# Performance work log

Measured on AMD Instinct MI355X. Metric: run time of the kernel, lower is better.

## Reference

```python
import jax, jax.numpy as jnp
import numpy as np

B, NC, C, H, L = 256, 99, 128, 512, 3
N = NC + 1              # nodes per graph (depot + customers)
NT = B * N              # total nodes
EPS = 1e-5


def _edge_index():
    # PyG-style: torch.combinations(arange(n), r=2) -> directed upper-tri edges, replicated per batch
    r, c = np.triu_indices(N, k=1)
    offs = (np.arange(B) * N)[:, None]
    row = (r[None, :] + offs).ravel()
    col = (c[None, :] + offs).ravel()
    # gcn_norm adds self loops
    sl = np.arange(NT)
    row = np.concatenate([row, sl])
    col = np.concatenate([col, sl])
    return jnp.asarray(row, jnp.int32), jnp.asarray(col, jnp.int32)


def _bn(x, g, b):
    # BatchNorm1d in training mode over flattened (B*n, C); biased variance
    m = x.mean(0)
    v = jnp.mean((x - m) ** 2, axis=0)
    return g * (x - m) * jax.lax.rsqrt(v + EPS) + b


def setup_inputs() -> dict:
    key = jax.random.key(0)
    ks = jax.random.split(key, 16)
    f = jax.random.normal
    return dict(
        depot_xy=jax.random.uniform(ks[0], (B, 2), jnp.float32),
        customer_xy=jax.random.uniform(ks[1], (B, NC, 2), jnp.float32),
        demand=jax.random.uniform(ks[2], (B, NC), jnp.float32),
        W_depot=f(ks[3], (2, C), jnp.float32) * 0.5,
        b_depot=f(ks[4], (C,), jnp.float32) * 0.1,
        W_init=f(ks[5], (3, C), jnp.float32) * 0.5,
        b_init=f(ks[6], (C,), jnp.float32) * 0.1,
        gcn_W=f(ks[7], (L, C, C), jnp.float32) / np.sqrt(C),
        gcn_b=f(ks[8], (L, C), jnp.float32) * 0.1,
        bn_gamma=jnp.ones((L, C), jnp.float32),
        bn_beta=jnp.zeros((L, C), jnp.float32),
        ff_W1=f(ks[9], (L, C, H), jnp.float32) / np.sqrt(C),
        ff_b1=f(ks[10], (L, H), jnp.float32) * 0.1,
        ff_W2=f(ks[11], (L, H, C), jnp.float32) / np.sqrt(H),
        ff_b2=f(ks[12], (L, C), jnp.float32) * 0.1,
    )


def reference(depot_xy, customer_xy, demand, W_depot, b_depot, W_init, b_init,
              gcn_W, gcn_b, bn_gamma, bn_beta, ff_W1, ff_b1, ff_W2, ff_b2):
    # initial node embeddings
    depot_e = depot_xy @ W_depot + b_depot                      # [B, C]
    cust_in = jnp.concatenate([customer_xy, demand[..., None]], -1)  # [B, NC, 3]
    cust_e = cust_in @ W_init + b_init                          # [B, NC, C]
    x = jnp.concatenate([depot_e[:, None, :], cust_e], 1).reshape(NT, C)

    row, col = _edge_index()
    # GCN symmetric normalization (with self loops, directed src->dst)
    deg = jax.ops.segment_sum(jnp.ones_like(col, x.dtype), col, num_segments=NT)
    dis = jnp.where(deg > 0, jax.lax.rsqrt(deg), 0.0)
    norm = dis[row] * dis[col]                                  # [E]

    for l in range(L):
        h = x @ gcn_W[l]                                        # [NT, C]
        msg = norm[:, None] * h[row]                            # gather + scale
        agg = jax.ops.segment_sum(msg, col, num_segments=NT) + gcn_b[l]
        x = _bn(x + agg, bn_gamma[l], bn_beta[l])
        ff = jax.nn.relu(x @ ff_W1[l] + ff_b1[l]) @ ff_W2[l] + ff_b2[l]
        x = _bn(x + ff, bn_gamma[l], bn_beta[l])

    nodes = x.reshape(B, N, C)
    return nodes, jnp.mean(nodes, axis=1)
```

## Files before the change

### kernel.cpp

```cpp
#include <hip/hip_runtime.h>

constexpr int kB = 256;
constexpr int kNC = 99;
constexpr int kN = 100;
constexpr int kC = 128;
constexpr int kH = 512;
constexpr int kL = 3;
constexpr int kNT = kB * kN;
constexpr int kRT = 64;
constexpr int kFFBlocks = kNT / kRT;
constexpr float kEps = 1e-5f;

typedef unsigned short u16;
typedef unsigned int u32;
typedef __attribute__((ext_vector_type(8))) __bf16 bf16x8;
typedef __attribute__((ext_vector_type(4))) float f32x4;
typedef __attribute__((ext_vector_type(8))) unsigned short u16x8;

__device__ __forceinline__ u16 f2bf(float x) {
  __bf16 h = (__bf16)x;
  return __builtin_bit_cast(u16, h);
}
__device__ __forceinline__ float bf2f(u16 h) {
  union { u32 u; float f; } v; v.u = ((u32)h) << 16;
  return v.f;
}

__device__ __forceinline__ void affine_from_stats(
    const float* __restrict__ stats, const float* __restrict__ gamma,
    const float* __restrict__ beta, int c, float& sc, float& sh) {
  if (stats != nullptr) {
    float s = stats[c], sq = stats[kC + c];
    float m = s * (1.0f / kNT);
    float v = sq * (1.0f / kNT) - m * m;
    float rs = rsqrtf(v + kEps);
    sc = gamma[c] * rs;
    sh = beta[c] - m * sc;
  } else {
    sc = 1.0f;
    sh = 0.0f;
  }
}

__device__ __forceinline__ void pack_group(
    int g, const float* __restrict__ gcnW, const float* __restrict__ W1,
    const float* __restrict__ W2, u16* __restrict__ wpack) {
  int layer = g / 36864, r = g % 36864;
  const float* src; int shf; u16* base; int isW2 = 0;
  if (r < 4096) {
    src = gcnW + (size_t)layer * kC * kC; shf = 7;
    base = wpack + (size_t)(layer * 288 + 0) * 512;
  } else if (r < 20480) {
    src = W1 + (size_t)layer * kC * kH; shf = 9;
    base = wpack + (size_t)(layer * 288 + 32) * 512; r -= 4096;
  } else {
    src = W2 + (size_t)layer * kH * kC; shf = 7;
    base = wpack + (size_t)(layer * 288 + 160) * 512; r -= 20480; isW2 = 1;
  }
  int e4 = r * 4;
  int k = e4 >> shf, n0 = e4 & ((1 << shf) - 1);
  float4 v = *(const float4*)(src + ((size_t)k << shf) + n0);
  float vv[4] = {v.x, v.y, v.z, v.w};
  int kb = k >> 5, hi = (k >> 3) & 3, j = k & 7;
#pragma unroll
  for (int t = 0; t < 4; ++t) {
    int n = n0 + t;
    int nb = n >> 4, l = hi * 16 + (n & 15);
    int f = isW2 ? (nb * 16 + kb) : (nb * 4 + kb);
    base[(size_t)f * 512 + l * 8 + j] = f2bf(vv[t]);
  }
}

template <bool FIRST>
__global__ __launch_bounds__(256) void k_gcn(
    const u16* __restrict__ yprev, const float* __restrict__ stats_prev,
    const float* __restrict__ gamma_p, const float* __restrict__ beta_p,
    const u16* __restrict__ Wgp, const float* __restrict__ gb,
    float* __restrict__ stats_out, u16* __restrict__ yA,
    const float* __restrict__ dxy, const float* __restrict__ cxy,
    const float* __restrict__ dem, const float* __restrict__ Wd,
    const float* __restrict__ bd, const float* __restrict__ Wi,
    const float* __restrict__ bi, const float* __restrict__ gcnW,
    const float* __restrict__ W1, const float* __restrict__ W2,
    u16* __restrict__ wpack) {
  __shared__ float s_scale[kC], s_shift[kC];
  __shared__ u16 xs[112][136];
  __shared__ float hs[kN][68];
  __shared__ float sP[4][64], s_sum[64], s_sq[64];
  __shared__ float scoord[kN][4];
  __shared__ float swt[7][kC];
  const int tid = threadIdx.x;
  const int b = blockIdx.x >> 1, half = blockIdx.x & 1;
  const int wave = tid >> 6, lane = tid & 63;
  const int arow = lane & 15, kofs = (lane >> 4) * 8;
  const int crow = (lane >> 4) * 4, ccol = lane & 15;
  const int nbW = half * 4 + wave;
  bf16x8 bfr[4];
  if (FIRST) {
#pragma unroll
    for (int kb = 0; kb < 4; ++kb)
#pragma unroll
      for (int e = 0; e < 8; ++e) {
        int krow = kb * 32 + (lane >> 4) * 8 + e;
        bfr[kb][e] = (__bf16)gcnW[(size_t)krow * kC + nbW * 16 + (lane & 15)];
      }
  } else {
#pragma unroll
    for (int kb = 0; kb < 4; ++kb)
      bfr[kb] = *(const bf16x8*)(Wgp + (size_t)(nbW * 4 + kb) * 512 + lane * 8);
  }
  if (FIRST) {
    int g = blockIdx.x * 256 + tid;
    if (g < kL * 36864) pack_group(g, gcnW, W1, W2, wpack);
    if (tid < kN) {
      if (tid == 0) {
        scoord[0][0] = dxy[b * 2];
        scoord[0][1] = dxy[b * 2 + 1];
        scoord[0][2] = 0.0f;
      } else {
        int q = b * kNC + tid - 1;
        scoord[tid][0] = cxy[q * 2];
        scoord[tid][1] = cxy[q * 2 + 1];
        scoord[tid][2] = dem[q];
      }
    }
    if (tid < 224) {
      int f = tid * 4, r = f >> 7, c = f & 127;
      const float* s;
      switch (r) {
        case 0: s = Wd + c; break;
        case 1: s = Wd + kC + c; break;
        case 2: s = bd + c; break;
        case 3: s = Wi + c; break;
        case 4: s = Wi + kC + c; break;
        case 5: s = Wi + 2 * kC + c; break;
        default: s = bi + c; break;
      }
      *(float4*)&swt[r][c] = *(const float4*)s;
    }
  }
  if (tid < kC) affine_from_stats(stats_prev, gamma_p, beta_p, tid,
                                  s_scale[tid], s_shift[tid]);
  if (tid < 64) { s_sum[tid] = 0.0f; s_sq[tid] = 0.0f; }
  __syncthreads();
  const size_t gbase = (size_t)b * kN * kC;
#pragma unroll
  for (int i = 0; i < 14; ++i) {
    int li = i * 256 + tid;
    int lr = li >> 5, lc = (li & 31) * 4;
    float g0 = 0.f, g1 = 0.f, g2 = 0.f, g3 = 0.f;
    if (lr < kN) {
      if (FIRST) {
        float sx = scoord[lr][0], sy = scoord[lr][1], sd = scoord[lr][2];
        if (lr == 0) {
          g0 = fmaf(sx, swt[0][lc + 0], fmaf(sy, swt[1][lc + 0], swt[2][lc + 0]));
          g1 = fmaf(sx, swt[0][lc + 1], fmaf(sy, swt[1][lc + 1], swt[2][lc + 1]));
          g2 = fmaf(sx, swt[0][lc + 2], fmaf(sy, swt[1][lc + 2], swt[2][lc + 2]));
          g3 = fmaf(sx, swt[0][lc + 3], fmaf(sy, swt[1][lc + 3], swt[2][lc + 3]));
        } else {
          g0 = fmaf(sx, swt[3][lc + 0],
                    fmaf(sy, swt[4][lc + 0], fmaf(sd, swt[5][lc + 0], swt[6][lc + 0])));
          g1 = fmaf(sx, swt[3][lc + 1],
                    fmaf(sy, swt[4][lc + 1], fmaf(sd, swt[5][lc + 1], swt[6][lc + 1])));
          g2 = fmaf(sx, swt[3][lc + 2],
                    fmaf(sy, swt[4][lc + 2], fmaf(sd, swt[5][lc + 2], swt[6][lc + 2])));
          g3 = fmaf(sx, swt[3][lc + 3],
                    fmaf(sy, swt[4][lc + 3], fmaf(sd, swt[5][lc + 3], swt[6][lc + 3])));
        }
      } else {
        ushort4 hv = *(const ushort4*)(yprev + gbase + (size_t)lr * kC + lc);
        g0 = bf2f(hv.x); g1 = bf2f(hv.y); g2 = bf2f(hv.z); g3 = bf2f(hv.w);
      }
    }
    ushort4 h4;
    h4.x = f2bf(fmaf(g0, s_scale[lc + 0], s_shift[lc + 0]));
    h4.y = f2bf(fmaf(g1, s_scale[lc + 1], s_shift[lc + 1]));
    h4.z = f2bf(fmaf(g2, s_scale[lc + 2], s_shift[lc + 2]));
    h4.w = f2bf(fmaf(g3, s_scale[lc + 3], s_shift[lc + 3]));
    *(ushort4*)&xs[lr][lc] = h4;
  }
  __syncthreads();
  {
#pragma unroll
    for (int t = 0; t < 7; ++t) {
      f32x4 acc = {0.f, 0.f, 0.f, 0.f};
#pragma unroll
      for (int kb = 0; kb < 4; ++kb) {
        bf16x8 a = *(const bf16x8*)&xs[t * 16 + arow][kb * 32 + kofs];
        acc = __builtin_amdgcn_mfma_f32_16x16x32_bf16(a, bfr[kb], acc, 0, 0, 0);
      }
      int rbase = t * 16 + crow;
#pragma unroll
      for (int r = 0; r < 4; ++r)
        if (rbase + r < kN) hs[rbase + r][wave * 16 + ccol] = acc[r];
    }
  }
  __syncthreads();
  const int c = tid & 63, jh = tid >> 6;
  const int ch = half * 64 + c;
  const float sc = s_scale[ch], sh = s_shift[ch];
  const float gbc = gb[ch];
  const int j0 = jh * 25;
  float p = 0.0f;
#pragma unroll
  for (int jj = 0; jj < 25; ++jj)
    p = fmaf(hs[j0 + jj][c], rsqrtf((float)(j0 + jj + 1)), p);
  sP[jh][c] = p;
  __syncthreads();
  float s = 0.0f;
  for (int q = 0; q < jh; ++q) s += sP[q][c];
  float wv0 = 0.f, wv1 = 0.f, wv2 = 0.f, wv3 = 0.f, wd0 = 0.f, wd1 = 0.f, wd2 = 0.f;
  if (FIRST) {
    wv0 = swt[3][ch]; wv1 = swt[4][ch]; wv2 = swt[5][ch]; wv3 = swt[6][ch];
    wd0 = swt[0][ch]; wd1 = swt[1][ch]; wd2 = swt[2][ch];
  }
  float lsum = 0.0f, lsq = 0.0f;
#pragma unroll
  for (int jj = 0; jj < 25; ++jj) {
    int j = j0 + jj;
    float r = rsqrtf((float)(j + 1));
    s = fmaf(hs[j][c], r, s);
    float xv;
    if (FIRST) {
      float sx = scoord[j][0], sy = scoord[j][1], sd = scoord[j][2];
      xv = (j == 0) ? fmaf(sx, wd0, fmaf(sy, wd1, wd2))
                    : fmaf(sx, wv0, fmaf(sy, wv1, fmaf(sd, wv2, wv3)));
    } else {
      xv = fmaf(bf2f(yprev[gbase + (size_t)j * kC + ch]), sc, sh);
    }
    float yv = xv + fmaf(s, r, gbc);
    yA[gbase + (size_t)j * kC + ch] = f2bf(yv);
    lsum += yv;
    lsq = fmaf(yv, yv, lsq);
  }
  atomicAdd(&s_sum[c], lsum);
  atomicAdd(&s_sq[c], lsq);
  __syncthreads();
  if (tid < 64) {
    atomicAdd(&stats_out[half * 64 + tid], s_sum[tid]);
    atomicAdd(&stats_out[kC + half * 64 + tid], s_sq[tid]);
  }
}

template <bool LAST>
__global__ __launch_bounds__(512, 2) void k_ff(
    const u16* __restrict__ yA, const float* __restrict__ stats_in,
    const float* __restrict__ gamma, const float* __restrict__ beta,
    const u16* __restrict__ W1p, const float* __restrict__ b1,
    const u16* __restrict__ W2p, const float* __restrict__ b2,
    float* __restrict__ stats_out, u16* __restrict__ yB16,
    float* __restrict__ yB32) {
  __shared__ float s_scale[kC], s_shift[kC], s_sum[kC], s_sq[kC];
  __shared__ float s_b1[kH];
  __shared__ u16 xs[kRT][136];
  __shared__ u16 hid[kRT][136];
  const int tid = threadIdx.x;
  const int wave = tid >> 6, lane = tid & 63;
  const int arow = lane & 15, kofs = (lane >> 4) * 8;
  const int crow = (lane >> 4) * 4, ccol = lane & 15;
  if (tid < kC) {
    affine_from_stats(stats_in, gamma, beta, tid, s_scale[tid], s_shift[tid]);
    s_sum[tid] = 0.0f;
    s_sq[tid] = 0.0f;
  }
  if (tid < 128) ((float4*)s_b1)[tid] = ((const float4*)b1)[tid];
  __syncthreads();
  const int rb = blockIdx.x * kRT;
#pragma unroll
  for (int i = 0; i < 2; ++i) {
    int li = i * 512 + tid;
    int lr = li >> 4, lc8 = (li & 15) * 8;
    u16x8 hv = *(const u16x8*)(yA + (size_t)(rb + lr) * kC + lc8);
    u16x8 o;
#pragma unroll
    for (int e = 0; e < 8; ++e)
      o[e] = f2bf(fmaf(bf2f(hv[e]), s_scale[lc8 + e], s_shift[lc8 + e]));
    *(u16x8*)&xs[lr][lc8] = o;
  }
  const int c = wave * 16 + ccol;
  u16 resid[16];
#pragma unroll
  for (int rt = 0; rt < 4; ++rt)
#pragma unroll
    for (int r = 0; r < 4; ++r)
      resid[rt * 4 + r] = yA[(size_t)(rb + rt * 16 + crow + r) * kC + c];
  __syncthreads();

  f32x4 oacc[4] = {{0.f, 0.f, 0.f, 0.f}, {0.f, 0.f, 0.f, 0.f},
                   {0.f, 0.f, 0.f, 0.f}, {0.f, 0.f, 0.f, 0.f}};
  for (int chk = 0; chk < 4; ++chk) {
    bf16x8 bw[4];
#pragma unroll
    for (int kb = 0; kb < 4; ++kb)
      bw[kb] = *(const bf16x8*)(W2p + (size_t)(wave * 16 + chk * 4 + kb) * 512 + lane * 8);
    const int nb = chk * 8 + wave;
    bf16x8 b1f[4];
#pragma unroll
    for (int kb = 0; kb < 4; ++kb)
      b1f[kb] = *(const bf16x8*)(W1p + (size_t)(nb * 4 + kb) * 512 + lane * 8);
    const float bbias = s_b1[chk * 128 + c];
#pragma unroll
    for (int rt = 0; rt < 4; ++rt) {
      f32x4 acc = {0.f, 0.f, 0.f, 0.f};
#pragma unroll
      for (int kb = 0; kb < 4; ++kb) {
        bf16x8 a = *(const bf16x8*)&xs[rt * 16 + arow][kb * 32 + kofs];
        acc = __builtin_amdgcn_mfma_f32_16x16x32_bf16(a, b1f[kb], acc, 0, 0, 0);
      }
#pragma unroll
      for (int r = 0; r < 4; ++r)
        hid[rt * 16 + crow + r][c] = f2bf(fmaxf(acc[r] + bbias, 0.0f));
    }
    __syncthreads();
#pragma unroll
    for (int kb = 0; kb < 4; ++kb) {
#pragma unroll
      for (int rt = 0; rt < 4; ++rt) {
        bf16x8 ha = *(const bf16x8*)&hid[rt * 16 + arow][kb * 32 + kofs];
        oacc[rt] = __builtin_amdgcn_mfma_f32_16x16x32_bf16(ha, bw[kb], oacc[rt], 0, 0, 0);
      }
    }
    __syncthreads();
  }

  const float sc = s_scale[c], sh = s_shift[c], bb = b2[c];
  float psum = 0.0f, psq = 0.0f;
#pragma unroll
  for (int rt = 0; rt < 4; ++rt) {
#pragma unroll
    for (int r = 0; r < 4; ++r) {
      int lrow = rt * 16 + crow + r;
      float xv = fmaf(bf2f(resid[rt * 4 + r]), sc, sh);
      float o = oacc[rt][r] + bb + xv;
      if (LAST)
        yB32[(size_t)(rb + lrow) * kC + c] = o;
      else
        yB16[(size_t)(rb + lrow) * kC + c] = f2bf(o);
      psum += o;
      psq = fmaf(o, o, psq);
    }
  }
  atomicAdd(&s_sum[c], psum);
  atomicAdd(&s_sq[c], psq);
  __syncthreads();
  if (tid < kC) {
    atomicAdd(&stats_out[tid], s_sum[tid]);
    atomicAdd(&stats_out[kC + tid], s_sq[tid]);
  }
}

__global__ __launch_bounds__(1024) void k_out(
    const float* __restrict__ yB, const float* __restrict__ stats,
    const float* __restrict__ gamma, const float* __restrict__ beta,
    float* __restrict__ out) {
  __shared__ float sP[8][kC];
  const int b = blockIdx.x;
  const int c = threadIdx.x & 127, jh = threadIdx.x >> 7;
  float sc, sh;
  affine_from_stats(stats, gamma, beta, c, sc, sh);
  const int j0 = (jh < 4) ? jh * 13 : 52 + (jh - 4) * 12;
  const int jc = (jh < 4) ? 13 : 12;
  float acc = 0.0f;
  const size_t base = (size_t)b * kN * kC + c;
  for (int jj = 0; jj < jc; ++jj) {
    int j = j0 + jj;
    float xv = fmaf(yB[base + (size_t)j * kC], sc, sh);
    out[base + (size_t)j * kC] = xv;
    acc += xv;
  }
  sP[jh][c] = acc;
  __syncthreads();
  if (jh == 0) {
    float m = 0.0f;
#pragma unroll
    for (int q = 0; q < 8; ++q) m += sP[q][c];
    out[(size_t)kNT * kC + (size_t)b * kC + c] = m * (1.0f / kN);
  }
}

extern "C" void kernel_launch(void* const* d_in, const int* in_sizes, int n_in,
                              void* d_out, int out_size, void* d_ws, size_t ws_size,
                              hipStream_t stream) {
  const float* depot_xy    = (const float*)d_in[0];
  const float* customer_xy = (const float*)d_in[1];
  const float* demand      = (const float*)d_in[2];
  const float* W_depot     = (const float*)d_in[3];
  const float* b_depot     = (const float*)d_in[4];
  const float* W_init      = (const float*)d_in[5];
  const float* b_init      = (const float*)d_in[6];
  const float* gcn_W       = (const float*)d_in[7];
  const float* gcn_b       = (const float*)d_in[8];
  const float* bn_gamma    = (const float*)d_in[9];
  const float* bn_beta     = (const float*)d_in[10];
  const float* ff_W1       = (const float*)d_in[11];
  const float* ff_b1       = (const float*)d_in[12];
  const float* ff_W2       = (const float*)d_in[13];
  const float* ff_b2       = (const float*)d_in[14];

  u16*   yA16  = (u16*)d_ws;
  u16*   yB16  = yA16 + (size_t)kNT * kC;
  float* yB32  = (float*)(yB16 + (size_t)kNT * kC);
  float* stats = yB32 + (size_t)kNT * kC;
  u16*   wpack = (u16*)(stats + kL * 2 * 2 * kC);

  hipMemsetAsync(stats, 0, kL * 2 * 2 * kC * sizeof(float), stream);
  for (int l = 0; l < kL; ++l) {
    const float* sp = (l == 0) ? nullptr : stats + ((l - 1) * 2 + 1) * 2 * kC;
    const float* gp = (l == 0) ? nullptr : bn_gamma + (l - 1) * kC;
    const float* bp = (l == 0) ? nullptr : bn_beta + (l - 1) * kC;
    float* s0 = stats + (l * 2 + 0) * 2 * kC;
    float* s1 = stats + (l * 2 + 1) * 2 * kC;
    const u16* wg  = wpack + (size_t)(l * 288 + 0) * 512;
    const u16* w1p = wpack + (size_t)(l * 288 + 32) * 512;
    const u16* w2p = wpack + (size_t)(l * 288 + 160) * 512;
    if (l == 0) {
      k_gcn<true><<<kB * 2, 256, 0, stream>>>(
          nullptr, sp, gp, bp, nullptr, gcn_b + l * kC, s0, yA16,
          depot_xy, customer_xy, demand, W_depot, b_depot, W_init, b_init,
          gcn_W, ff_W1, ff_W2, wpack);
    } else {
      k_gcn<false><<<kB * 2, 256, 0, stream>>>(
          yB16, sp, gp, bp, wg, gcn_b + l * kC, s0, yA16,
          nullptr, nullptr, nullptr, nullptr, nullptr, nullptr, nullptr,
          nullptr, nullptr, nullptr, nullptr);
    }
    if (l < kL - 1) {
      k_ff<false><<<kFFBlocks, 512, 0, stream>>>(
          yA16, s0, bn_gamma + l * kC, bn_beta + l * kC,
          w1p, ff_b1 + l * kH, w2p, ff_b2 + l * kC, s1, yB16, nullptr);
    } else {
      k_ff<true><<<kFFBlocks, 512, 0, stream>>>(
          yA16, s0, bn_gamma + l * kC, bn_beta + l * kC,
          w1p, ff_b1 + l * kH, w2p, ff_b2 + l * kC, s1, nullptr, yB32);
    }
  }
  k_out<<<kB, 1024, 0, stream>>>(yB32, stats + (2 * 2 + 1) * 2 * kC,
                                 bn_gamma + 2 * kC, bn_beta + 2 * kC, (float*)d_out);
}
```

Before: 129.4 us.

## Alias GCN LDS buffers, widen FF hidden chunks, raise occupancy bounds

```diff
diff --git a/kernel.cpp b/kernel.cpp
--- a/kernel.cpp
+++ b/kernel.cpp
@@ -72,7 +72,7 @@
 }
 
 template <bool FIRST>
-__global__ __launch_bounds__(256) void k_gcn(
+__global__ __launch_bounds__(256, 4) void k_gcn(
     const u16* __restrict__ yprev, const float* __restrict__ stats_prev,
     const float* __restrict__ gamma_p, const float* __restrict__ beta_p,
     const u16* __restrict__ Wgp, const float* __restrict__ gb,
@@ -84,11 +84,12 @@
     const float* __restrict__ W1, const float* __restrict__ W2,
     u16* __restrict__ wpack) {
   __shared__ float s_scale[kC], s_shift[kC];
-  __shared__ u16 xs[112][136];
-  __shared__ float hs[kN][68];
+  __shared__ __align__(16) u16 ubuf[112 * 136];
   __shared__ float sP[4][64], s_sum[64], s_sq[64];
   __shared__ float scoord[kN][4];
   __shared__ float swt[7][kC];
+  u16 (*xs)[136] = (u16(*)[136])ubuf;
+  float* hs = (float*)ubuf;
   const int tid = threadIdx.x;
   const int b = blockIdx.x >> 1, half = blockIdx.x & 1;
   const int wave = tid >> 6, lane = tid & 63;
@@ -145,55 +146,48 @@
   __syncthreads();
   const size_t gbase = (size_t)b * kN * kC;
 #pragma unroll
-  for (int i = 0; i < 14; ++i) {
+  for (int i = 0; i < 7; ++i) {
     int li = i * 256 + tid;
-    int lr = li >> 5, lc = (li & 31) * 4;
-    float g0 = 0.f, g1 = 0.f, g2 = 0.f, g3 = 0.f;
+    int lr = li >> 4, lc8 = (li & 15) * 8;
+    u16x8 o = {0, 0, 0, 0, 0, 0, 0, 0};
     if (lr < kN) {
       if (FIRST) {
         float sx = scoord[lr][0], sy = scoord[lr][1], sd = scoord[lr][2];
-        if (lr == 0) {
-          g0 = fmaf(sx, swt[0][lc + 0], fmaf(sy, swt[1][lc + 0], swt[2][lc + 0]));
-          g1 = fmaf(sx, swt[0][lc + 1], fmaf(sy, swt[1][lc + 1], swt[2][lc + 1]));
-          g2 = fmaf(sx, swt[0][lc + 2], fmaf(sy, swt[1][lc + 2], swt[2][lc + 2]));
-          g3 = fmaf(sx, swt[0][lc + 3], fmaf(sy, swt[1][lc + 3], swt[2][lc + 3]));
-        } else {
-          g0 = fmaf(sx, swt[3][lc + 0],
-                    fmaf(sy, swt[4][lc + 0], fmaf(sd, swt[5][lc + 0], swt[6][lc + 0])));
-          g1 = fmaf(sx, swt[3][lc + 1],
-                    fmaf(sy, swt[4][lc + 1], fmaf(sd, swt[5][lc + 1], swt[6][lc + 1])));
-          g2 = fmaf(sx, swt[3][lc + 2],
-                    fmaf(sy, swt[4][lc + 2], fmaf(sd, swt[5][lc + 2], swt[6][lc + 2])));
-          g3 = fmaf(sx, swt[3][lc + 3],
-                    fmaf(sy, swt[4][lc + 3], fmaf(sd, swt[5][lc + 3], swt[6][lc + 3])));
+#pragma unroll
+        for (int e = 0; e < 8; ++e) {
+          int c = lc8 + e;
+          float g = (lr == 0)
+              ? fmaf(sx, swt[0][c], fmaf(sy, swt[1][c], swt[2][c]))
+              : fmaf(sx, swt[3][c], fmaf(sy, swt[4][c], fmaf(sd, swt[5][c], swt[6][c])));
+          o[e] = f2bf(fmaf(g, s_scale[c], s_shift[c]));
         }
       } else {
-        ushort4 hv = *(const ushort4*)(yprev + gbase + (size_t)lr * kC + lc);
-        g0 = bf2f(hv.x); g1 = bf2f(hv.y); g2 = bf2f(hv.z); g3 = bf2f(hv.w);
-      }
-    }
-    ushort4 h4;
-    h4.x = f2bf(fmaf(g0, s_scale[lc + 0], s_shift[lc + 0]));
-    h4.y = f2bf(fmaf(g1, s_scale[lc + 1], s_shift[lc + 1]));
-    h4.z = f2bf(fmaf(g2, s_scale[lc + 2], s_shift[lc + 2]));
-    h4.w = f2bf(fmaf(g3, s_scale[lc + 3], s_shift[lc + 3]));
-    *(ushort4*)&xs[lr][lc] = h4;
-  }
-  __syncthreads();
-  {
-#pragma unroll
-    for (int t = 0; t < 7; ++t) {
-      f32x4 acc = {0.f, 0.f, 0.f, 0.f};
-#pragma unroll
-      for (int kb = 0; kb < 4; ++kb) {
-        bf16x8 a = *(const bf16x8*)&xs[t * 16 + arow][kb * 32 + kofs];
-        acc = __builtin_amdgcn_mfma_f32_16x16x32_bf16(a, bfr[kb], acc, 0, 0, 0);
-      }
-      int rbase = t * 16 + crow;
-#pragma unroll
-      for (int r = 0; r < 4; ++r)
-        if (rbase + r < kN) hs[rbase + r][wave * 16 + ccol] = acc[r];
-    }
+        u16x8 hv = *(const u16x8*)(yprev + gbase + (size_t)lr * kC + lc8);
+#pragma unroll
+        for (int e = 0; e < 8; ++e)
+          o[e] = f2bf(fmaf(bf2f(hv[e]), s_scale[lc8 + e], s_shift[lc8 + e]));
+      }
+    }
+    *(u16x8*)&xs[lr][lc8] = o;
+  }
+  __syncthreads();
+  f32x4 acc[7];
+#pragma unroll
+  for (int t = 0; t < 7; ++t) {
+    acc[t] = {0.f, 0.f, 0.f, 0.f};
+#pragma unroll
+    for (int kb = 0; kb < 4; ++kb) {
+      bf16x8 a = *(const bf16x8*)&xs[t * 16 + arow][kb * 32 + kofs];
+      acc[t] = __builtin_amdgcn_mfma_f32_16x16x32_bf16(a, bfr[kb], acc[t], 0, 0, 0);
+    }
+  }
+  __syncthreads();
+#pragma unroll
+  for (int t = 0; t < 7; ++t) {
+    int rbase = t * 16 + crow;
+#pragma unroll
+    for (int r = 0; r < 4; ++r)
+      if (rbase + r < kN) hs[(rbase + r) * 68 + wave * 16 + ccol] = acc[t][r];
   }
   __syncthreads();
   const int c = tid & 63, jh = tid >> 6;
@@ -204,7 +198,7 @@
   float p = 0.0f;
 #pragma unroll
   for (int jj = 0; jj < 25; ++jj)
-    p = fmaf(hs[j0 + jj][c], rsqrtf((float)(j0 + jj + 1)), p);
+    p = fmaf(hs[(j0 + jj) * 68 + c], rsqrtf((float)(j0 + jj + 1)), p);
   sP[jh][c] = p;
   __syncthreads();
   float s = 0.0f;
@@ -219,7 +213,7 @@
   for (int jj = 0; jj < 25; ++jj) {
     int j = j0 + jj;
     float r = rsqrtf((float)(j + 1));
-    s = fmaf(hs[j][c], r, s);
+    s = fmaf(hs[j * 68 + c], r, s);
     float xv;
     if (FIRST) {
       float sx = scoord[j][0], sy = scoord[j][1], sd = scoord[j][2];
@@ -243,7 +237,7 @@
 }
 
 template <bool LAST>
-__global__ __launch_bounds__(512, 2) void k_ff(
+__global__ __launch_bounds__(512, 4) void k_ff(
     const u16* __restrict__ yA, const float* __restrict__ stats_in,
     const float* __restrict__ gamma, const float* __restrict__ beta,
     const u16* __restrict__ W1p, const float* __restrict__ b1,
@@ -253,7 +247,7 @@
   __shared__ float s_scale[kC], s_shift[kC], s_sum[kC], s_sq[kC];
   __shared__ float s_b1[kH];
   __shared__ u16 xs[kRT][136];
-  __shared__ u16 hid[kRT][136];
+  __shared__ u16 hid[kRT][272];
   const int tid = threadIdx.x;
   const int wave = tid >> 6, lane = tid & 63;
   const int arow = lane & 15, kofs = (lane >> 4) * 8;
@@ -288,36 +282,40 @@
 
   f32x4 oacc[4] = {{0.f, 0.f, 0.f, 0.f}, {0.f, 0.f, 0.f, 0.f},
                    {0.f, 0.f, 0.f, 0.f}, {0.f, 0.f, 0.f, 0.f}};
-  for (int chk = 0; chk < 4; ++chk) {
-    bf16x8 bw[4];
-#pragma unroll
-    for (int kb = 0; kb < 4; ++kb)
-      bw[kb] = *(const bf16x8*)(W2p + (size_t)(wave * 16 + chk * 4 + kb) * 512 + lane * 8);
-    const int nb = chk * 8 + wave;
-    bf16x8 b1f[4];
-#pragma unroll
-    for (int kb = 0; kb < 4; ++kb)
-      b1f[kb] = *(const bf16x8*)(W1p + (size_t)(nb * 4 + kb) * 512 + lane * 8);
-    const float bbias = s_b1[chk * 128 + c];
-#pragma unroll
-    for (int rt = 0; rt < 4; ++rt) {
-      f32x4 acc = {0.f, 0.f, 0.f, 0.f};
-#pragma unroll
-      for (int kb = 0; kb < 4; ++kb) {
-        bf16x8 a = *(const bf16x8*)&xs[rt * 16 + arow][kb * 32 + kofs];
-        acc = __builtin_amdgcn_mfma_f32_16x16x32_bf16(a, b1f[kb], acc, 0, 0, 0);
-      }
-#pragma unroll
-      for (int r = 0; r < 4; ++r)
-        hid[rt * 16 + crow + r][c] = f2bf(fmaxf(acc[r] + bbias, 0.0f));
+  for (int chk = 0; chk < 2; ++chk) {
+    bf16x8 bw[8];
+#pragma unroll
+    for (int kk = 0; kk < 8; ++kk)
+      bw[kk] = *(const bf16x8*)(W2p + (size_t)(wave * 16 + chk * 8 + kk) * 512 + lane * 8);
+#pragma unroll
+    for (int q = 0; q < 2; ++q) {
+      const int nb = chk * 16 + wave * 2 + q;
+      bf16x8 b1f[4];
+#pragma unroll
+      for (int kb = 0; kb < 4; ++kb)
+        b1f[kb] = *(const bf16x8*)(W1p + (size_t)(nb * 4 + kb) * 512 + lane * 8);
+      const int cl = (wave * 2 + q) * 16 + ccol;
+      const float bbias = s_b1[chk * 256 + cl];
+#pragma unroll
+      for (int rt = 0; rt < 4; ++rt) {
+        f32x4 acc = {0.f, 0.f, 0.f, 0.f};
+#pragma unroll
+        for (int kb = 0; kb < 4; ++kb) {
+          bf16x8 a = *(const bf16x8*)&xs[rt * 16 + arow][kb * 32 + kofs];
+          acc = __builtin_amdgcn_mfma_f32_16x16x32_bf16(a, b1f[kb], acc, 0, 0, 0);
+        }
+#pragma unroll
+        for (int r = 0; r < 4; ++r)
+          hid[rt * 16 + crow + r][cl] = f2bf(fmaxf(acc[r] + bbias, 0.0f));
+      }
     }
     __syncthreads();
 #pragma unroll
-    for (int kb = 0; kb < 4; ++kb) {
+    for (int kk = 0; kk < 8; ++kk) {
 #pragma unroll
       for (int rt = 0; rt < 4; ++rt) {
-        bf16x8 ha = *(const bf16x8*)&hid[rt * 16 + arow][kb * 32 + kofs];
-        oacc[rt] = __builtin_amdgcn_mfma_f32_16x16x32_bf16(ha, bw[kb], oacc[rt], 0, 0, 0);
+        bf16x8 ha = *(const bf16x8*)&hid[rt * 16 + arow][kk * 32 + kofs];
+        oacc[rt] = __builtin_amdgcn_mfma_f32_16x16x32_bf16(ha, bw[kk], oacc[rt], 0, 0, 0);
       }
     }
     __syncthreads();
```

Measured after the change: 126.8 us. About the same (-2.0%).
